# Performance work log

Hardware: AMD Instinct MI355X
Metric: run time of the kernel (lower is better)

## Reference

```python
import jax, jax.numpy as jnp
import numpy as np

HIDDEN = 2048
N_HEADS = 32
N_KV_HEADS = 4
HEAD_DIM = 128
N_REP = N_HEADS // N_KV_HEADS
D_FF = 8192
ROPE_BASE = 1000000.0
MROPE_SECTIONS = [48, 40, 40]  # mrope_section [24,20,20] doubled; sums to HEAD_DIM
EPS = 1e-6


def rms_norm(x, w, eps=EPS):
    var = jnp.mean(x * x, axis=-1, keepdims=True)
    return w * (x * jax.lax.rsqrt(var + eps))


def mrope_cos_sin(seq_len):
    # MultimodalRotaryEmbedding: per-section inv_freq, emb = cat(freqs, freqs).
    # All 3 position types use the same t = arange(seq_len) here, so the
    # section-interleaved selection (chunk i from type i%3) collapses to a
    # single (seq, HEAD_DIM) table with layout [f0 f0 | f1 f1 | f2 f2].
    t = jnp.arange(seq_len, dtype=jnp.float32)
    cos_parts, sin_parts = [], []
    for sd in MROPE_SECTIONS:
        inv_freq = 1.0 / (ROPE_BASE ** (jnp.arange(0, sd, 2, dtype=jnp.float32) / sd))
        freqs = jnp.outer(t, inv_freq)               # (S, sd/2)
        emb = jnp.concatenate([freqs, freqs], -1)    # (S, sd)
        cos_parts.append(jnp.cos(emb))
        sin_parts.append(jnp.sin(emb))
    cos = jnp.concatenate(cos_parts, -1)  # (S, HEAD_DIM)
    sin = jnp.concatenate(sin_parts, -1)
    return cos[None, None], sin[None, None]  # (1,1,S,D)


def rotate_half(x):
    d = x.shape[-1] // 2
    return jnp.concatenate([-x[..., d:], x[..., :d]], -1)


def setup_inputs() -> dict:
    key = jax.random.key(0)
    ks = jax.random.split(key, 12)
    B, S = 2, 2048
    x = jax.random.normal(ks[0], (B, S, HIDDEN), jnp.float32)
    causal = jnp.tril(jnp.ones((S, S), jnp.bool_))
    attention_mask = jnp.where(causal, 0.0, -1e9).astype(jnp.float32)
    attention_mask = jnp.broadcast_to(attention_mask[None, None], (B, 1, S, S))
    sc = 0.02
    return {
        "x": x,
        "attention_mask": attention_mask,
        "wq": jax.random.normal(ks[1], (N_HEADS * HEAD_DIM, HIDDEN), jnp.float32) * sc,
        "wk": jax.random.normal(ks[2], (N_KV_HEADS * HEAD_DIM, HIDDEN), jnp.float32) * sc,
        "wv": jax.random.normal(ks[3], (N_KV_HEADS * HEAD_DIM, HIDDEN), jnp.float32) * sc,
        "wo": jax.random.normal(ks[4], (HIDDEN, N_HEADS * HEAD_DIM), jnp.float32) * sc,
        "q_norm_w": jnp.ones((HEAD_DIM,), jnp.float32),
        "k_norm_w": jnp.ones((HEAD_DIM,), jnp.float32),
        "ln1_w": jnp.ones((HIDDEN,), jnp.float32),
        "ln2_w": jnp.ones((HIDDEN,), jnp.float32),
        "w_gate": jax.random.normal(ks[5], (D_FF, HIDDEN), jnp.float32) * sc,
        "w_up": jax.random.normal(ks[6], (D_FF, HIDDEN), jnp.float32) * sc,
        "w_down": jax.random.normal(ks[7], (HIDDEN, D_FF), jnp.float32) * sc,
    }


def attention(h, mask, wq, wk, wv, wo, q_norm_w, k_norm_w):
    B, S, _ = h.shape
    q = (h @ wq.T).reshape(B, S, N_HEADS, HEAD_DIM).transpose(0, 2, 1, 3)       # (B,H,S,D)
    k = (h @ wk.T).reshape(B, S, N_KV_HEADS, HEAD_DIM).transpose(0, 2, 1, 3)    # (B,Hkv,S,D)
    v = (h @ wv.T).reshape(B, S, N_KV_HEADS, HEAD_DIM).transpose(0, 2, 1, 3)
    # per-head QK RMSNorm
    q = rms_norm(q, q_norm_w)
    k = rms_norm(k, k_norm_w)
    # mRoPE
    cos, sin = mrope_cos_sin(S)
    q = q * cos + rotate_half(q) * sin
    k = k * cos + rotate_half(k) * sin
    # GQA: repeat KV heads to match Q heads
    k = jnp.repeat(k, N_REP, axis=1)
    v = jnp.repeat(v, N_REP, axis=1)
    scores = jnp.einsum("bhqd,bhkd->bhqk", q, k) / np.sqrt(HEAD_DIM)
    scores = scores + mask
    probs = jax.nn.softmax(scores.astype(jnp.float32), axis=-1).astype(q.dtype)
    out = jnp.einsum("bhqk,bhkd->bhqd", probs, v)
    out = out.transpose(0, 2, 1, 3).reshape(B, S, N_HEADS * HEAD_DIM)
    return out @ wo.T


def mlp(h, w_gate, w_up, w_down):
    return (jax.nn.silu(h @ w_gate.T) * (h @ w_up.T)) @ w_down.T


def reference(x, attention_mask, wq, wk, wv, wo, q_norm_w, k_norm_w,
              ln1_w, ln2_w, w_gate, w_up, w_down):
    h = x + attention(rms_norm(x, ln1_w), attention_mask,
                      wq, wk, wv, wo, q_norm_w, k_norm_w)
    out = h + mlp(rms_norm(h, ln2_w), w_gate, w_up, w_down)
    return out
```

## Files before the change

### kernel.cpp

```cpp
#include <hip/hip_runtime.h>
#include <hip/hip_bf16.h>

typedef __attribute__((ext_vector_type(4))) float f32x4;
typedef __attribute__((ext_vector_type(8))) short short8;
using uint = unsigned int;
using ushort = unsigned short;

#define DEV __device__ __forceinline__

DEV ushort f2bf(float f) {
  uint u = __builtin_bit_cast(uint, f);
  u = (u + 0x7fffu + ((u >> 16) & 1u)) >> 16;
  return (ushort)u;
}
DEV float bf2f(ushort b) { uint u = ((uint)b) << 16; return __builtin_bit_cast(float, u); }
DEV uint pack2(float lo, float hi) { return (uint)f2bf(lo) | ((uint)f2bf(hi) << 16); }

DEV void gll16(const ushort* g, ushort* l) {
  __builtin_amdgcn_global_load_lds((const __attribute__((address_space(1))) void*)g,
                                   (__attribute__((address_space(3))) void*)l, 16, 0, 0);
}

#define MFMA_BF16 __builtin_amdgcn_mfma_f32_16x16x32_bf16

__global__ __launch_bounds__(256) void cast_bf16_k(const float* __restrict__ src, ushort* __restrict__ dst) {
  size_t i = ((size_t)blockIdx.x * 256 + threadIdx.x) * 8;
  float4 a = *(const float4*)(src + i);
  float4 b = *(const float4*)(src + i + 4);
  uint4 u;
  u.x = pack2(a.x, a.y); u.y = pack2(a.z, a.w);
  u.z = pack2(b.x, b.y); u.w = pack2(b.z, b.w);
  *(uint4*)(dst + i) = u;
}

__global__ __launch_bounds__(256) void rope_table_k(float* __restrict__ cost, float* __restrict__ sint) {
  int idx = blockIdx.x * 256 + threadIdx.x;
  int s = idx >> 7, d = idx & 127;
  const float LN1E6 = 13.815510557964274f;
  float inv;
  if (d < 48)      { int i = d % 24;        inv = expf((float)i * (-2.f / 48.f) * LN1E6); }
  else if (d < 88) { int i = (d - 48) % 20; inv = expf((float)i * (-2.f / 40.f) * LN1E6); }
  else             { int i = (d - 88) % 20; inv = expf((float)i * (-2.f / 40.f) * LN1E6); }
  float ang = (float)s * inv;
  cost[idx] = cosf(ang);
  sint[idx] = sinf(ang);
}

__global__ __launch_bounds__(256) void rmsnorm_k(const float* __restrict__ in, const float* __restrict__ w,
                                                 ushort* __restrict__ out) {
  int row = blockIdx.x;
  const float* x = in + (size_t)row * 2048;
  int base = threadIdx.x * 8;
  float4 a = *(const float4*)(x + base);
  float4 b = *(const float4*)(x + base + 4);
  float ss = a.x*a.x + a.y*a.y + a.z*a.z + a.w*a.w + b.x*b.x + b.y*b.y + b.z*b.z + b.w*b.w;
#pragma unroll
  for (int msk = 1; msk <= 32; msk <<= 1) ss += __shfl_xor(ss, msk);
  __shared__ float red[4];
  if ((threadIdx.x & 63) == 0) red[threadIdx.x >> 6] = ss;
  __syncthreads();
  float tot = red[0] + red[1] + red[2] + red[3];
  float r = rsqrtf(tot * (1.f / 2048.f) + 1e-6f);
  float4 wa = *(const float4*)(w + base);
  float4 wb = *(const float4*)(w + base + 4);
  uint4 u;
  u.x = pack2(a.x * r * wa.x, a.y * r * wa.y);
  u.y = pack2(a.z * r * wa.z, a.w * r * wa.w);
  u.z = pack2(b.x * r * wb.x, b.y * r * wb.y);
  u.w = pack2(b.z * r * wb.z, b.w * r * wb.w);
  *(uint4*)(out + (size_t)row * 2048 + base) = u;
}

template <int MODE, int SUPER>
__global__ __launch_bounds__(256, 4) void gemm_bb(
    const ushort* __restrict__ A, int lda,
    const ushort* __restrict__ B, int ldb,
    ushort* __restrict__ Cb, float* __restrict__ Cf,
    const float* __restrict__ resid, int ldc, int K) {
  __shared__ ushort smem[2 * 128 * 64];
  ushort* As = smem;
  ushort* Bs = smem + 128 * 64;

  int tid = threadIdx.x;
  int w = tid >> 6, lane = tid & 63, g = lane >> 4, c = lane & 15;
  int wr = w >> 1, wc = w & 1;

  int gx = gridDim.x;
  int nwg = gx * gridDim.y;
  int id = blockIdx.y * gx + blockIdx.x;
  int cpx = nwg >> 3;
  int id2 = (id & 7) * cpx + (id >> 3);
  int m0, n0;
  if (SUPER) {
    int sgx = gx >> 3;
    int s = id2 >> 6, w2 = id2 & 63;
    m0 = ((s / sgx) * 8 + (w2 >> 3)) * 128;
    n0 = ((s % sgx) * 8 + (w2 & 7)) * 128;
  } else {
    m0 = (id2 / gx) * 128;
    n0 = (id2 % gx) * 128;
  }

  f32x4 acc[4][4] = {};

  int srow8 = lane >> 3;
  int scol = ((lane & 7) ^ srow8) * 8;
  const ushort* Ab = A + (size_t)(m0 + w * 32 + srow8) * lda + scol;
  const ushort* Bb = B + (size_t)(n0 + w * 32 + srow8) * ldb + scol;
  ushort* AsW = As + (w * 32) * 64;
  ushort* BsW = Bs + (w * 32) * 64;

  for (int k0 = 0; k0 < K; k0 += 64) {
#pragma unroll
    for (int i = 0; i < 4; ++i) {
      gll16(Ab + (size_t)i * 8 * lda + k0, AsW + i * 8 * 64);
      gll16(Bb + (size_t)i * 8 * ldb + k0, BsW + i * 8 * 64);
    }
    __syncthreads();
#pragma unroll
    for (int kk = 0; kk < 2; ++kk) {
      short8 af[4], bf4[4];
#pragma unroll
      for (int mi = 0; mi < 4; ++mi)
        af[mi] = *(const short8*)(&As[(wr * 64 + mi * 16 + c) * 64 + (((kk * 4 + g) ^ (c & 7))) * 8]);
#pragma unroll
      for (int ni = 0; ni < 4; ++ni)
        bf4[ni] = *(const short8*)(&Bs[(wc * 64 + ni * 16 + c) * 64 + (((kk * 4 + g) ^ (c & 7))) * 8]);
#pragma unroll
      for (int mi = 0; mi < 4; ++mi)
#pragma unroll
        for (int ni = 0; ni < 4; ++ni)
          acc[mi][ni] = MFMA_BF16(af[mi], bf4[ni], acc[mi][ni], 0, 0, 0);
    }
    __syncthreads();
  }

  float* eps = (float*)smem;
  float* my = eps + w * (16 * 68);
  int erow = lane >> 2;
  int ecl = (lane & 3) * 16;
#pragma unroll
  for (int mi = 0; mi < 4; ++mi) {
#pragma unroll
    for (int ni = 0; ni < 4; ++ni)
#pragma unroll
      for (int r = 0; r < 4; ++r)
        my[(g * 4 + r) * 68 + ni * 16 + c] = acc[mi][ni][r];
    int grow = m0 + wr * 64 + mi * 16 + erow;
    int gcol = n0 + wc * 64 + ecl;
    float4 t0 = *(float4*)(&my[erow * 68 + ecl + 0]);
    float4 t1 = *(float4*)(&my[erow * 68 + ecl + 4]);
    float4 t2 = *(float4*)(&my[erow * 68 + ecl + 8]);
    float4 t3 = *(float4*)(&my[erow * 68 + ecl + 12]);
    size_t off = (size_t)grow * ldc + gcol;
    if (MODE == 1) {
      float4 r0 = *(const float4*)(resid + off + 0);
      float4 r1 = *(const float4*)(resid + off + 4);
      float4 r2 = *(const float4*)(resid + off + 8);
      float4 r3 = *(const float4*)(resid + off + 12);
      t0.x += r0.x; t0.y += r0.y; t0.z += r0.z; t0.w += r0.w;
      t1.x += r1.x; t1.y += r1.y; t1.z += r1.z; t1.w += r1.w;
      t2.x += r2.x; t2.y += r2.y; t2.z += r2.z; t2.w += r2.w;
      t3.x += r3.x; t3.y += r3.y; t3.z += r3.z; t3.w += r3.w;
      *(float4*)(Cf + off + 0) = t0;
      *(float4*)(Cf + off + 4) = t1;
      *(float4*)(Cf + off + 8) = t2;
      *(float4*)(Cf + off + 12) = t3;
    } else if (MODE == 0) {
      uint4 u0, u1;
      u0.x = pack2(t0.x, t0.y); u0.y = pack2(t0.z, t0.w);
      u0.z = pack2(t1.x, t1.y); u0.w = pack2(t1.z, t1.w);
      u1.x = pack2(t2.x, t2.y); u1.y = pack2(t2.z, t2.w);
      u1.z = pack2(t3.x, t3.y); u1.w = pack2(t3.z, t3.w);
      *(uint4*)(Cb + off) = u0;
      *(uint4*)(Cb + off + 8) = u1;
    } else {
      uint4 g0 = *(const uint4*)(Cb + off);
      uint4 g1 = *(const uint4*)(Cb + off + 8);
      uint gw[8] = {g0.x, g0.y, g0.z, g0.w, g1.x, g1.y, g1.z, g1.w};
      float tv[16] = {t0.x, t0.y, t0.z, t0.w, t1.x, t1.y, t1.z, t1.w,
                      t2.x, t2.y, t2.z, t2.w, t3.x, t3.y, t3.z, t3.w};
      float ov[16];
#pragma unroll
      for (int j = 0; j < 8; ++j) {
        float ga = bf2f((ushort)(gw[j] & 0xffff));
        float gb = bf2f((ushort)(gw[j] >> 16));
        ov[2 * j]     = ga / (1.f + __expf(-ga)) * tv[2 * j];
        ov[2 * j + 1] = gb / (1.f + __expf(-gb)) * tv[2 * j + 1];
      }
      uint4 u0, u1;
      u0.x = pack2(ov[0], ov[1]);   u0.y = pack2(ov[2], ov[3]);
      u0.z = pack2(ov[4], ov[5]);   u0.w = pack2(ov[6], ov[7]);
      u1.x = pack2(ov[8], ov[9]);   u1.y = pack2(ov[10], ov[11]);
      u1.z = pack2(ov[12], ov[13]); u1.w = pack2(ov[14], ov[15]);
      *(uint4*)(Cb + off) = u0;
      *(uint4*)(Cb + off + 8) = u1;
    }
  }
}

__global__ __launch_bounds__(256) void qk_rope_k(ushort* __restrict__ qkv,
                                                 const float* __restrict__ qw, const float* __restrict__ kw,
                                                 const float* __restrict__ cost, const float* __restrict__ sint) {
  int row = blockIdx.x;
  int s = row & 2047;
  int w = threadIdx.x >> 6, l = threadIdx.x & 63;
  ushort* rp = qkv + (size_t)row * 5120;
  float c0 = cost[s * 128 + l], c1 = cost[s * 128 + l + 64];
  float s0 = sint[s * 128 + l], s1 = sint[s * 128 + l + 64];
  float qw0 = qw[l], qw1 = qw[l + 64];
  float kw0 = kw[l], kw1 = kw[l + 64];
#pragma unroll
  for (int i = 0; i < 9; ++i) {
    int hd = w + 4 * i;
    bool isq = hd < 32;
    int colbase = isq ? hd * 128 : 4096 + (hd - 32) * 128;
    ushort* p = rp + colbase;
    float x0 = bf2f(p[l]), x1 = bf2f(p[l + 64]);
    float ss = x0 * x0 + x1 * x1;
#pragma unroll
    for (int msk = 1; msk <= 32; msk <<= 1) ss += __shfl_xor(ss, msk);
    float r = rsqrtf(ss * (1.f / 128.f) + 1e-6f);
    float xn0 = x0 * r * (isq ? qw0 : kw0);
    float xn1 = x1 * r * (isq ? qw1 : kw1);
    float v0 = xn0 * c0 - xn1 * s0;
    float v1 = xn1 * c1 + xn0 * s1;
    if (isq) { v0 *= 0.08838834764831843f; v1 *= 0.08838834764831843f; }
    p[l] = f2bf(v0);
    p[l + 64] = f2bf(v1);
  }
}

__global__ __launch_bounds__(256) void transpose_v_k(const ushort* __restrict__ qkv, ushort* __restrict__ vT) {
  __shared__ ushort Ls[128 * 72];
  int st = blockIdx.x, kvh = blockIdx.y, b = blockIdx.z;
  int t = threadIdx.x;
  int s0 = st * 64;
  const ushort* src = qkv + (size_t)(b * 2048) * 5120 + 4608 + kvh * 128;
#pragma unroll
  for (int i = 0; i < 4; ++i) {
    int sl = i * 16 + (t >> 4);
    int d0 = (t & 15) * 8;
    short8 v = *(const short8*)(src + (size_t)(s0 + sl) * 5120 + d0);
#pragma unroll
    for (int j = 0; j < 8; ++j) Ls[(d0 + j) * 72 + sl] = (ushort)v[j];
  }
  __syncthreads();
  int d = t >> 1, half = t & 1;
  ushort* dst = vT + (size_t)(b * 4 + kvh) * 128 * 2048 + (size_t)d * 2048 + s0 + half * 32;
#pragma unroll
  for (int j = 0; j < 4; ++j)
    *(uint4*)(dst + j * 8) = *(uint4*)(&Ls[d * 72 + half * 32 + j * 8]);
}

__global__ __launch_bounds__(256, 2) void attn_k(const ushort* __restrict__ qkv,
                                                 const ushort* __restrict__ vT,
                                                 ushort* __restrict__ outp) {
  __shared__ ushort Ks[2][16 * 512];
  __shared__ ushort Vs[2][16 * 512];
  __shared__ ushort Ps[4][2][1024];

  int hp = blockIdx.y, b = blockIdx.z;
  int h0 = hp * 2;
  int kvh = h0 >> 3;
  int tid = threadIdx.x, w = tid >> 6, l = tid & 63, g = l >> 4, c = l & 15;

  const ushort* kbase = qkv + (size_t)(b * 2048) * 5120 + 4096 + kvh * 128;
  const ushort* vbase = vT + (size_t)(b * 4 + kvh) * 128 * 2048;

  int krow = l & 15, kcol = (l >> 4) * 8;

  auto stage = [&](int t, int buf) {
    int kv0 = t * 64;
#pragma unroll
    for (int kk = 0; kk < 4; ++kk)
      gll16(kbase + (size_t)(kv0 + w * 16 + krow) * 5120 + kk * 32 + kcol,
            &Ks[buf][(kk * 4 + w) * 512]);
#pragma unroll
    for (int i = 0; i < 4; ++i) {
      int kk = i >> 1, db = 2 * w + (i & 1);
      gll16(vbase + (size_t)(db * 16 + krow) * 2048 + kv0 + kk * 32 + kcol,
            &Vs[buf][(kk * 8 + db) * 512]);
    }
  };

#pragma unroll 1
  for (int pass = 0; pass < 2; ++pass) {
    int qt = pass == 0 ? (31 - (int)blockIdx.x) : (int)blockIdx.x;
    int qrow = qt * 64 + w * 16 + c;

    short8 qf0[4], qf1[4];
    const ushort* qp = qkv + (size_t)(b * 2048 + qrow) * 5120 + h0 * 128 + g * 8;
#pragma unroll
    for (int kk = 0; kk < 4; ++kk) {
      qf0[kk] = *(const short8*)(qp + kk * 32);
      qf1[kk] = *(const short8*)(qp + 128 + kk * 32);
    }

    f32x4 o0[8] = {}, o1[8] = {};
    float rmax0 = -1e30f, lsum0 = 0.f, rmax1 = -1e30f, lsum1 = 0.f;

    auto do_softmax = [&](f32x4 sfr[4], float& rmax, float& lsum, ushort* pdst,
                          int kv0, bool need_mask) {
      float sv[16];
      float tmax = -3e38f;
#pragma unroll
      for (int f = 0; f < 4; ++f)
#pragma unroll
        for (int r = 0; r < 4; ++r) {
          int key = kv0 + f * 16 + g * 4 + r;
          float xv = sfr[f][r];
          if (need_mask) xv += (key > qrow) ? -1e9f : 0.f;
          sv[f * 4 + r] = xv;
          tmax = fmaxf(tmax, xv);
        }
      tmax = fmaxf(tmax, __shfl_xor(tmax, 16));
      tmax = fmaxf(tmax, __shfl_xor(tmax, 32));
      float mnew, alpha;
      if (__all(tmax - rmax <= 8.0f)) {
        mnew = rmax;
        alpha = 1.0f;
      } else {
        mnew = fmaxf(rmax, tmax);
        alpha = __expf(rmax - mnew);
      }
      float psum = 0.f;
      uint pw[8];
#pragma unroll
      for (int i = 0; i < 16; i += 2) {
        float p0 = __expf(sv[i] - mnew);
        float p1 = __expf(sv[i + 1] - mnew);
        psum += p0 + p1;
        pw[i >> 1] = pack2(p0, p1);
      }
      psum += __shfl_xor(psum, 16);
      psum += __shfl_xor(psum, 32);
      lsum = lsum * alpha + psum;
      rmax = mnew;
#pragma unroll
      for (int f = 0; f < 4; ++f)
        *(uint2*)(pdst + (f >> 1) * 512 + (c + 16 * ((f & 1) * 2 + (g >> 1))) * 8 + (g & 1) * 4) =
            make_uint2(pw[2 * f], pw[2 * f + 1]);
      return alpha;
    };

    int nt = qt + 1;
    stage(0, 0);
    for (int t = 0; t < nt; ++t) {
      int cur = t & 1;
      int kv0 = t * 64;
      if (t + 1 < nt) {
        stage(t + 1, cur ^ 1);
        asm volatile("s_waitcnt vmcnt(8)" ::: "memory");
      } else {
        asm volatile("s_waitcnt vmcnt(0)" ::: "memory");
      }
      __builtin_amdgcn_sched_barrier(0);
      __builtin_amdgcn_s_barrier();

      f32x4 s0[4] = {}, s1[4] = {};
      __builtin_amdgcn_s_setprio(1);
#pragma unroll
      for (int kk = 0; kk < 4; ++kk)
#pragma unroll
        for (int f = 0; f < 4; ++f) {
          short8 kf = *(const short8*)(&Ks[cur][(kk * 4 + f) * 512 + l * 8]);
          s0[f] = MFMA_BF16(kf, qf0[kk], s0[f], 0, 0, 0);
          s1[f] = MFMA_BF16(kf, qf1[kk], s1[f], 0, 0, 0);
        }
      __builtin_amdgcn_s_setprio(0);

      bool need_mask = (t == qt);
      float alpha0 = do_softmax(s0, rmax0, lsum0, &Ps[w][0][0], kv0, need_mask);
      float alpha1 = do_softmax(s1, rmax1, lsum1, &Ps[w][1][0], kv0, need_mask);

      if (alpha0 != 1.0f || alpha1 != 1.0f) {
#pragma unroll
        for (int db = 0; db < 8; ++db) {
          o0[db][0] *= alpha0; o0[db][1] *= alpha0; o0[db][2] *= alpha0; o0[db][3] *= alpha0;
          o1[db][0] *= alpha1; o1[db][1] *= alpha1; o1[db][2] *= alpha1; o1[db][3] *= alpha1;
        }
      }

      __builtin_amdgcn_s_setprio(1);
#pragma unroll
      for (int kk = 0; kk < 2; ++kk) {
        short8 pf0 = *(const short8*)(&Ps[w][0][kk * 512 + l * 8]);
        short8 pf1 = *(const short8*)(&Ps[w][1][kk * 512 + l * 8]);
#pragma unroll
        for (int db = 0; db < 8; ++db) {
          short8 vf = *(const short8*)(&Vs[cur][(kk * 8 + db) * 512 + l * 8]);
          o0[db] = MFMA_BF16(vf, pf0, o0[db], 0, 0, 0);
          o1[db] = MFMA_BF16(vf, pf1, o1[db], 0, 0, 0);
        }
      }
      __builtin_amdgcn_s_setprio(0);
      __builtin_amdgcn_s_barrier();
    }

    float inv0 = 1.0f / lsum0, inv1 = 1.0f / lsum1;
    size_t rowoff = (size_t)(b * 2048 + qrow) * 4096 + h0 * 128;
#pragma unroll
    for (int db = 0; db < 8; ++db) {
      *(uint2*)(outp + rowoff + db * 16 + g * 4) =
          make_uint2(pack2(o0[db][0] * inv0, o0[db][1] * inv0), pack2(o0[db][2] * inv0, o0[db][3] * inv0));
      *(uint2*)(outp + rowoff + 128 + db * 16 + g * 4) =
          make_uint2(pack2(o1[db][0] * inv1, o1[db][1] * inv1), pack2(o1[db][2] * inv1, o1[db][3] * inv1));
    }
  }
}

extern "C" void kernel_launch(void* const* d_in, const int* in_sizes, int n_in,
                              void* d_out, int out_size, void* d_ws, size_t ws_size,
                              hipStream_t stream) {
  const float* x   = (const float*)d_in[0];
  const float* wq  = (const float*)d_in[2];
  const float* wk  = (const float*)d_in[3];
  const float* wv  = (const float*)d_in[4];
  const float* wo  = (const float*)d_in[5];
  const float* qnw = (const float*)d_in[6];
  const float* knw = (const float*)d_in[7];
  const float* ln1 = (const float*)d_in[8];
  const float* ln2 = (const float*)d_in[9];
  const float* wg  = (const float*)d_in[10];
  const float* wu  = (const float*)d_in[11];
  const float* wd  = (const float*)d_in[12];
  float* outp = (float*)d_out;

  char* ws = (char*)d_ws;
  ushort* wqkv_bf = (ushort*)ws; ws += (size_t)5120 * 2048 * 2;
  ushort* wo_bf   = (ushort*)ws; ws += (size_t)2048 * 4096 * 2;
  ushort* wg_bf   = (ushort*)ws; ws += (size_t)8192 * 2048 * 2;
  ushort* wu_bf   = (ushort*)ws; ws += (size_t)8192 * 2048 * 2;
  ushort* wd_bf   = (ushort*)ws; ws += (size_t)2048 * 8192 * 2;
  float*  cost    = (float*)ws;  ws += (size_t)2048 * 128 * 4;
  float*  sint    = (float*)ws;  ws += (size_t)2048 * 128 * 4;
  ushort* h1      = (ushort*)ws; ws += (size_t)4096 * 2048 * 2;
  ushort* h2      = h1;
  ushort* qkv     = (ushort*)ws;
  ushort* vT      = qkv + (size_t)4096 * 5120;
  ushort* atn     = vT + (size_t)8 * 128 * 2048;
  ushort* gate    = qkv;

  cast_bf16_k<<<4096, 256, 0, stream>>>(wq, wqkv_bf);
  cast_bf16_k<<<512,  256, 0, stream>>>(wk, wqkv_bf + (size_t)4096 * 2048);
  cast_bf16_k<<<512,  256, 0, stream>>>(wv, wqkv_bf + (size_t)4608 * 2048);
  cast_bf16_k<<<4096, 256, 0, stream>>>(wo, wo_bf);
  cast_bf16_k<<<8192, 256, 0, stream>>>(wg, wg_bf);
  cast_bf16_k<<<8192, 256, 0, stream>>>(wu, wu_bf);
  cast_bf16_k<<<8192, 256, 0, stream>>>(wd, wd_bf);

  rope_table_k<<<1024, 256, 0, stream>>>(cost, sint);
  rmsnorm_k<<<4096, 256, 0, stream>>>(x, ln1, h1);

  gemm_bb<0, 1><<<dim3(40, 32), 256, 0, stream>>>(h1, 2048, wqkv_bf, 2048, qkv, nullptr, nullptr, 5120, 2048);

  qk_rope_k<<<4096, 256, 0, stream>>>(qkv, qnw, knw, cost, sint);
  transpose_v_k<<<dim3(32, 4, 2), 256, 0, stream>>>(qkv, vT);
  attn_k<<<dim3(16, 16, 2), 256, 0, stream>>>(qkv, vT, atn);

  gemm_bb<1, 0><<<dim3(16, 32), 256, 0, stream>>>(atn, 4096, wo_bf, 4096, nullptr, outp, x, 2048, 4096);

  rmsnorm_k<<<4096, 256, 0, stream>>>(outp, ln2, h2);
  gemm_bb<0, 1><<<dim3(64, 32), 256, 0, stream>>>(h2, 2048, wg_bf, 2048, gate, nullptr, nullptr, 8192, 2048);
  gemm_bb<2, 1><<<dim3(64, 32), 256, 0, stream>>>(h2, 2048, wu_bf, 2048, gate, nullptr, nullptr, 8192, 2048);
  gemm_bb<1, 0><<<dim3(16, 32), 256, 0, stream>>>(gate, 8192, wd_bf, 8192, nullptr, outp, outp, 2048, 8192);
}
```

Baseline: 890.2 us.

## Fuse gate and up projections into one GEMM with SiLU epilogue

Replaces the two separate gate and up GEMMs, the second of which re-read the gate output to apply SiLU, with one kernel. It loads a single A tile and two B tiles per K step and keeps gate and up accumulators side by side. The SiLU-multiply happens in the epilogue before a single bf16 store. This removes one full pass over the activation matrix and the gate intermediate's write and re-read. In exchange it uses more registers per thread, has a smaller 128x64 output tile, and adds a grid-swizzle mapping.

```diff
diff --git a/kernel.cpp b/kernel.cpp
--- a/kernel.cpp
+++ b/kernel.cpp
@@ -166,7 +166,7 @@
       *(float4*)(Cf + off + 4) = t1;
       *(float4*)(Cf + off + 8) = t2;
       *(float4*)(Cf + off + 12) = t3;
-    } else if (MODE == 0) {
+    } else {
       uint4 u0, u1;
       u0.x = pack2(t0.x, t0.y); u0.y = pack2(t0.z, t0.w);
       u0.z = pack2(t1.x, t1.y); u0.w = pack2(t1.z, t1.w);
@@ -174,28 +174,98 @@
       u1.z = pack2(t3.x, t3.y); u1.w = pack2(t3.z, t3.w);
       *(uint4*)(Cb + off) = u0;
       *(uint4*)(Cb + off + 8) = u1;
-    } else {
-      uint4 g0 = *(const uint4*)(Cb + off);
-      uint4 g1 = *(const uint4*)(Cb + off + 8);
-      uint gw[8] = {g0.x, g0.y, g0.z, g0.w, g1.x, g1.y, g1.z, g1.w};
-      float tv[16] = {t0.x, t0.y, t0.z, t0.w, t1.x, t1.y, t1.z, t1.w,
-                      t2.x, t2.y, t2.z, t2.w, t3.x, t3.y, t3.z, t3.w};
-      float ov[16];
-#pragma unroll
-      for (int j = 0; j < 8; ++j) {
-        float ga = bf2f((ushort)(gw[j] & 0xffff));
-        float gb = bf2f((ushort)(gw[j] >> 16));
-        ov[2 * j]     = ga / (1.f + __expf(-ga)) * tv[2 * j];
-        ov[2 * j + 1] = gb / (1.f + __expf(-gb)) * tv[2 * j + 1];
-      }
-      uint4 u0, u1;
-      u0.x = pack2(ov[0], ov[1]);   u0.y = pack2(ov[2], ov[3]);
-      u0.z = pack2(ov[4], ov[5]);   u0.w = pack2(ov[6], ov[7]);
-      u1.x = pack2(ov[8], ov[9]);   u1.y = pack2(ov[10], ov[11]);
-      u1.z = pack2(ov[12], ov[13]); u1.w = pack2(ov[14], ov[15]);
-      *(uint4*)(Cb + off) = u0;
-      *(uint4*)(Cb + off + 8) = u1;
-    }
+    }
+  }
+}
+
+__global__ __launch_bounds__(256, 4) void gemm_gu(
+    const ushort* __restrict__ A, int lda,
+    const ushort* __restrict__ Bg, const ushort* __restrict__ Bu, int ldb,
+    ushort* __restrict__ Cb, int ldc, int K) {
+  __shared__ ushort smem[2 * 128 * 64];
+  ushort* As = smem;
+  ushort* Bsg = smem + 128 * 64;
+  ushort* Bsu = smem + 128 * 64 + 64 * 64;
+
+  int tid = threadIdx.x;
+  int w = tid >> 6, lane = tid & 63, g = lane >> 4, c = lane & 15;
+  int wr = w >> 1, wc = w & 1;
+
+  int gx = gridDim.x;
+  int nwg = gx * gridDim.y;
+  int id = blockIdx.y * gx + blockIdx.x;
+  int cpx = nwg >> 3;
+  int id2 = (id & 7) * cpx + (id >> 3);
+  int sgx = gx >> 3;
+  int s = id2 >> 6, w2 = id2 & 63;
+  int m0 = ((s / sgx) * 8 + (w2 >> 3)) * 128;
+  int n0 = ((s % sgx) * 8 + (w2 & 7)) * 64;
+
+  f32x4 accg[4][2] = {}, accu[4][2] = {};
+
+  int srow8 = lane >> 3;
+  int scol = ((lane & 7) ^ srow8) * 8;
+  const ushort* Ab  = A  + (size_t)(m0 + w * 32 + srow8) * lda + scol;
+  const ushort* Bgb = Bg + (size_t)(n0 + w * 16 + srow8) * ldb + scol;
+  const ushort* Bub = Bu + (size_t)(n0 + w * 16 + srow8) * ldb + scol;
+  ushort* AsW  = As  + (w * 32) * 64;
+  ushort* BsgW = Bsg + (w * 16) * 64;
+  ushort* BsuW = Bsu + (w * 16) * 64;
+
+  for (int k0 = 0; k0 < K; k0 += 64) {
+#pragma unroll
+    for (int i = 0; i < 4; ++i)
+      gll16(Ab + (size_t)i * 8 * lda + k0, AsW + i * 8 * 64);
+#pragma unroll
+    for (int i = 0; i < 2; ++i) {
+      gll16(Bgb + (size_t)i * 8 * ldb + k0, BsgW + i * 8 * 64);
+      gll16(Bub + (size_t)i * 8 * ldb + k0, BsuW + i * 8 * 64);
+    }
+    __syncthreads();
+#pragma unroll
+    for (int kk = 0; kk < 2; ++kk) {
+      int co = (((kk * 4 + g) ^ (c & 7))) * 8;
+      short8 af[4], bg2[2], bu2[2];
+#pragma unroll
+      for (int mi = 0; mi < 4; ++mi)
+        af[mi] = *(const short8*)(&As[(wr * 64 + mi * 16 + c) * 64 + co]);
+#pragma unroll
+      for (int ni = 0; ni < 2; ++ni) {
+        bg2[ni] = *(const short8*)(&Bsg[(wc * 32 + ni * 16 + c) * 64 + co]);
+        bu2[ni] = *(const short8*)(&Bsu[(wc * 32 + ni * 16 + c) * 64 + co]);
+      }
+#pragma unroll
+      for (int mi = 0; mi < 4; ++mi)
+#pragma unroll
+        for (int ni = 0; ni < 2; ++ni) {
+          accg[mi][ni] = MFMA_BF16(af[mi], bg2[ni], accg[mi][ni], 0, 0, 0);
+          accu[mi][ni] = MFMA_BF16(af[mi], bu2[ni], accu[mi][ni], 0, 0, 0);
+        }
+    }
+    __syncthreads();
+  }
+
+  float* eps = (float*)smem;
+  float* my = eps + w * (16 * 68);
+  int erow = lane >> 2;
+  int ecl = (lane & 3) * 8;
+#pragma unroll
+  for (int mi = 0; mi < 4; ++mi) {
+#pragma unroll
+    for (int ni = 0; ni < 2; ++ni)
+#pragma unroll
+      for (int r = 0; r < 4; ++r) {
+        float gv = accg[mi][ni][r], uv = accu[mi][ni][r];
+        my[(g * 4 + r) * 68 + ni * 16 + c] = gv / (1.f + __expf(-gv)) * uv;
+      }
+    int grow = m0 + wr * 64 + mi * 16 + erow;
+    int gcol = n0 + wc * 32 + ecl;
+    float4 t0 = *(float4*)(&my[erow * 68 + ecl + 0]);
+    float4 t1 = *(float4*)(&my[erow * 68 + ecl + 4]);
+    uint4 u;
+    u.x = pack2(t0.x, t0.y); u.y = pack2(t0.z, t0.w);
+    u.z = pack2(t1.x, t1.y); u.w = pack2(t1.z, t1.w);
+    *(uint4*)(Cb + (size_t)grow * ldc + gcol) = u;
   }
 }
 
@@ -462,7 +532,6 @@
   gemm_bb<1, 0><<<dim3(16, 32), 256, 0, stream>>>(atn, 4096, wo_bf, 4096, nullptr, outp, x, 2048, 4096);
 
   rmsnorm_k<<<4096, 256, 0, stream>>>(outp, ln2, h2);
-  gemm_bb<0, 1><<<dim3(64, 32), 256, 0, stream>>>(h2, 2048, wg_bf, 2048, gate, nullptr, nullptr, 8192, 2048);
-  gemm_bb<2, 1><<<dim3(64, 32), 256, 0, stream>>>(h2, 2048, wu_bf, 2048, gate, nullptr, nullptr, 8192, 2048);
+  gemm_gu<<<dim3(128, 32), 256, 0, stream>>>(h2, 2048, wg_bf, wu_bf, 2048, gate, 8192, 2048);
   gemm_bb<1, 0><<<dim3(16, 32), 256, 0, stream>>>(gate, 8192, wd_bf, 8192, nullptr, outp, outp, 2048, 8192);
 }
```

New measurement: 862.8 us, median of 2. 1.03x faster.
